# Optimization experiments

Measured on AMD Instinct MI355X. Metric: run time of the kernel, lower is better.

The kernel has to match this reference:

```python
import jax, jax.numpy as jnp
import numpy as np

N_NODES = 100000
IN_FEAT, HID, OUT_FEAT, GRID = 128, 64, 40, 8
N_EDGES = 1600000


def spmm(row, col, w, x):
    # out[i] = sum_{e: row[e]==i} w[e] * x[col[e]]
    return jax.ops.segment_sum(w[:, None] * x[col], row, num_segments=N_NODES)


def kan_layer(x, coeff):
    # coeff: [2, out, in, grid]; Fourier KAN: y[b,j] = sum_{i,k} cos(k x_bi) C0[j,i,k] + sin(k x_bi) C1[j,i,k]
    grid = coeff.shape[-1]
    k = jnp.arange(1, grid + 1, dtype=x.dtype)  # [G]
    ang = x[:, :, None] * k  # [N, in, G]
    y = jnp.einsum('bik,jik->bj', jnp.cos(ang), coeff[0])
    y = y + jnp.einsum('bik,jik->bj', jnp.sin(ang), coeff[1])
    return y


def setup_inputs() -> dict:
    key = jax.random.key(0)
    ks = jax.random.split(key, 8)
    scale = 1.0 / (np.sqrt(HID) * np.sqrt(GRID))
    return {
        'x': jax.random.normal(ks[0], (N_NODES, IN_FEAT), dtype=jnp.float32),
        'edge_row': jax.random.randint(ks[1], (N_EDGES,), 0, N_NODES),
        'edge_col': jax.random.randint(ks[2], (N_EDGES,), 0, N_NODES),
        'edge_weight': jax.random.uniform(ks[3], (N_EDGES,), dtype=jnp.float32),
        'W_in': jax.random.normal(ks[4], (IN_FEAT, HID), dtype=jnp.float32) / np.sqrt(IN_FEAT),
        'b_in': jnp.zeros((HID,), dtype=jnp.float32),
        'coeffs1': jax.random.normal(ks[5], (2, HID, HID, GRID), dtype=jnp.float32) * scale,
        'coeffs2': jax.random.normal(ks[6], (2, HID, HID, GRID), dtype=jnp.float32) * scale,
        'W_out': jax.random.normal(ks[7], (HID, OUT_FEAT), dtype=jnp.float32) / np.sqrt(HID),
    }


def reference(x, edge_row, edge_col, edge_weight, W_in, b_in, coeffs1, coeffs2, W_out):
    h = x @ W_in + b_in                                  # lin_in
    h = kan_layer(spmm(edge_row, edge_col, edge_weight, h), coeffs1)
    h = kan_layer(spmm(edge_row, edge_col, edge_weight, h), coeffs2)
    out = h @ W_out                                      # final bias-free linear
    return jax.nn.log_softmax(out, axis=-1)
```

## Files before the change

kernel.cpp:

```cpp
#include <hip/hip_runtime.h>
#include <hip/hip_bf16.h>
#include <string.h>


#define N_NODES 100000
#define IN_FEAT 128
#define HID 64
#define OUT_FEAT 40
#define NGRID 8
#define N_EDGES 1600000
#define NELEM (N_NODES * HID)

#define NB 98
#define CAP 18432
#define BCHUNK 4096
#define BIN_BLOCKS ((N_EDGES + BCHUNK - 1) / BCHUNK)
#define NTILES ((N_NODES + 63) / 64)

using short8 = __attribute__((ext_vector_type(8))) short;
using floatx4 = __attribute__((ext_vector_type(4))) float;
using uintx4 = __attribute__((ext_vector_type(4))) unsigned;

#define GLOAD_LDS16(gp, lp)                                                   \
  __builtin_amdgcn_global_load_lds(                                           \
      (const __attribute__((address_space(1))) unsigned*)(gp),                \
      (__attribute__((address_space(3))) unsigned*)(lp), 16, 0, 0)

__device__ __forceinline__ unsigned pack_bf16x2(float c, float s) {
  unsigned uc = __float_as_uint(c);
  unsigned us = __float_as_uint(s);
  uc += 0x7fffu + ((uc >> 16) & 1u);
  us += 0x7fffu + ((us >> 16) & 1u);
  return (uc >> 16) | (us & 0xffff0000u);
}

__device__ __forceinline__ unsigned cvtpk_bf16x2(float c, float s) {
  __hip_bfloat162 p = __float22bfloat162_rn(make_float2(c, s));
  unsigned r;
  memcpy(&r, &p, 4);
  return r;
}

__global__ __launch_bounds__(256) void prep_kernel(
    const float* __restrict__ x, const float* __restrict__ W,
    const float* __restrict__ b, float* __restrict__ h,
    const float* __restrict__ c1, const float* __restrict__ c2,
    unsigned* __restrict__ Brep1, unsigned* __restrict__ Brep2,
    int* __restrict__ btail) {
  __shared__ __align__(16) float xs[16 * IN_FEAT];
  int t = threadIdx.x;
  int nb = blockIdx.x;
  if (nb < 6250) {
    const float4* xsrc = (const float4*)(x + (size_t)nb * 16 * IN_FEAT);
    float4* xd = (float4*)xs;
    xd[t] = xsrc[t];
    xd[t + 256] = xsrc[t + 256];
    __syncthreads();
    int lane = t & 63, wv = t >> 6;
    float bj = b[lane];
    float a0 = bj, a1 = bj, a2 = bj, a3 = bj;
    const float* xr = xs + wv * 4 * IN_FEAT;
    const float* Wj = W + lane;
#pragma unroll 4
    for (int i4 = 0; i4 < 32; i4++) {
      float4 x0 = *(const float4*)(xr + 0 * IN_FEAT + i4 * 4);
      float4 x1 = *(const float4*)(xr + 1 * IN_FEAT + i4 * 4);
      float4 x2 = *(const float4*)(xr + 2 * IN_FEAT + i4 * 4);
      float4 x3 = *(const float4*)(xr + 3 * IN_FEAT + i4 * 4);
      float w0 = Wj[(i4 * 4 + 0) * HID];
      float w1 = Wj[(i4 * 4 + 1) * HID];
      float w2 = Wj[(i4 * 4 + 2) * HID];
      float w3 = Wj[(i4 * 4 + 3) * HID];
      a0 = fmaf(x0.x, w0, a0); a0 = fmaf(x0.y, w1, a0); a0 = fmaf(x0.z, w2, a0); a0 = fmaf(x0.w, w3, a0);
      a1 = fmaf(x1.x, w0, a1); a1 = fmaf(x1.y, w1, a1); a1 = fmaf(x1.z, w2, a1); a1 = fmaf(x1.w, w3, a1);
      a2 = fmaf(x2.x, w0, a2); a2 = fmaf(x2.y, w1, a2); a2 = fmaf(x2.z, w2, a2); a2 = fmaf(x2.w, w3, a2);
      a3 = fmaf(x3.x, w0, a3); a3 = fmaf(x3.y, w1, a3); a3 = fmaf(x3.z, w2, a3); a3 = fmaf(x3.w, w3, a3);
    }
    size_t nbase = (size_t)nb * 16 + wv * 4;
    h[(nbase + 0) * HID + lane] = a0;
    h[(nbase + 1) * HID + lane] = a1;
    h[(nbase + 2) * HID + lane] = a2;
    h[(nbase + 3) * HID + lane] = a3;
  } else if (nb < 6506) {
    int rb = nb - 6250;
    const float* coeffs = (rb < 128) ? c1 : c2;
    unsigned* Brep = (rb < 128) ? Brep1 : Brep2;
    int idx = (rb & 127) * 256 + t;
    int ch = idx >> 13;
    int rem = idx & 8191;
    int blk = rem >> 8;
    int jt = blk >> 3, ks = blk & 7;
    int rem2 = rem & 255;
    int ls = rem2 >> 2;
    int quad = ls >> 4, m_n = ls & 15;
    int jj = rem2 & 3;
    int j = jt * 16 + m_n;
    int r = ks >> 1, km1 = ((ks & 1) << 2) | jj;
    int i = ch * 16 + quad * 4 + r;
    int ws = i * 8 + km1;
    float cc0 = coeffs[(size_t)j * 512 + ws];
    float cc1 = coeffs[32768 + (size_t)j * 512 + ws];
    Brep[idx] = pack_bf16x2(cc0, cc1);
  } else {
    if (t < NB) btail[t] = t * CAP;
  }
}

__global__ __launch_bounds__(256) void bin_kernel(
    const int* __restrict__ row, const int* __restrict__ col,
    const float* __restrict__ w, int* __restrict__ btail,
    uint2* __restrict__ pack1) {
  __shared__ __align__(16) uint2 stage[BCHUNK];
  __shared__ int bcnt[NB];
  __shared__ int lbase[NB];
  __shared__ int gbase[NB];
  __shared__ int lcur[NB];
  __shared__ int sc[128];
  int t = threadIdx.x;
  int e0 = blockIdx.x * BCHUNK;
  if (t < NB) bcnt[t] = 0;
  __syncthreads();
  int rloc[16];
#pragma unroll
  for (int q = 0; q < 16; q++) {
    int e = e0 + q * 256 + t;
    int r = (e < N_EDGES) ? row[e] : -1;
    rloc[q] = r;
    if (r >= 0) atomicAdd(&bcnt[r >> 10], 1);
  }
  __syncthreads();
  int c = (t < NB) ? bcnt[t] : 0;
  if (t < 128) sc[t] = c;
  __syncthreads();
  int v = c;
#pragma unroll
  for (int off = 1; off < 128; off <<= 1) {
    int add = (t >= off && t < 128) ? sc[t - off] : 0;
    __syncthreads();
    if (t < 128) sc[t] = v = v + add;
    __syncthreads();
  }
  if (t < NB) {
    lbase[t] = v - c;
    lcur[t] = v - c;
    gbase[t] = atomicAdd(&btail[t], c);
  }
  __syncthreads();
#pragma unroll
  for (int q = 0; q < 16; q++) {
    int e = e0 + q * 256 + t;
    int r = rloc[q];
    if (r >= 0) {
      int p = atomicAdd(&lcur[r >> 10], 1);
      unsigned key = ((unsigned)(r & 1023) << 17) | (unsigned)col[e];
      stage[p] = make_uint2(key, __float_as_uint(w[e]));
    }
  }
  __syncthreads();
  int wv = t >> 6, lane = t & 63;
  for (int b = wv; b < NB; b += 4) {
    int len = bcnt[b], src = lbase[b];
    uint2* dst = pack1 + (size_t)gbase[b];
    for (int i = lane; i < len; i += 64)
      dst[i] = stage[src + i];
  }
}

__global__ __launch_bounds__(256) void bucket_finalize_kernel(
    const int* __restrict__ btail, const uint2* __restrict__ pack1,
    int* __restrict__ rowptr, uint2* __restrict__ pack2) {
  __shared__ int rcnt[1024];
  __shared__ int sc[256];
  __shared__ int binfo[2];
  int b = blockIdx.x, t = threadIdx.x;
  if (t < NB) sc[t] = btail[t] - t * CAP;
  rcnt[t] = 0; rcnt[t + 256] = 0; rcnt[t + 512] = 0; rcnt[t + 768] = 0;
  __syncthreads();
  if (t == 0) {
    int base = 0;
    for (int i = 0; i < b; i++) base += sc[i];
    binfo[0] = base;
    binfo[1] = sc[b];
  }
  __syncthreads();
  int base = binfo[0], len = binfo[1];
  const uint2* rec = pack1 + (size_t)b * CAP;
  for (int i = t; i < len; i += 256)
    atomicAdd(&rcnt[rec[i].x >> 17], 1);
  __syncthreads();
  int c0 = rcnt[4 * t], c1 = rcnt[4 * t + 1], c2 = rcnt[4 * t + 2], c3 = rcnt[4 * t + 3];
  int s4 = c0 + c1 + c2 + c3;
  sc[t] = s4;
  __syncthreads();
  int v = s4;
#pragma unroll
  for (int off = 1; off < 256; off <<= 1) {
    int add = (t >= off) ? sc[t - off] : 0;
    __syncthreads();
    sc[t] = v = v + add;
    __syncthreads();
  }
  int excl = v - s4;
  int p0 = base + excl;
  int p1 = p0 + c0, p2 = p1 + c1, p3 = p2 + c2;
  int r0 = (b << 10) + 4 * t;
  if (r0 + 0 < N_NODES) rowptr[r0 + 0] = p0;
  if (r0 + 1 < N_NODES) rowptr[r0 + 1] = p1;
  if (r0 + 2 < N_NODES) rowptr[r0 + 2] = p2;
  if (r0 + 3 < N_NODES) rowptr[r0 + 3] = p3;
  rcnt[4 * t] = p0; rcnt[4 * t + 1] = p1; rcnt[4 * t + 2] = p2; rcnt[4 * t + 3] = p3;
  __syncthreads();
  for (int i = t; i < len; i += 256) {
    uint2 p = rec[i];
    int pos = atomicAdd(&rcnt[p.x >> 17], 1);
    pack2[pos] = make_uint2(p.x & 0x1FFFFu, p.y);
  }
  if (b == NB - 1 && t == 0) rowptr[N_NODES] = N_EDGES;
}

template <int DO_FINAL>
__global__ __launch_bounds__(256, 4) void fused_spmm_kan_kernel(
    const int* __restrict__ rowptr, const uint2* __restrict__ pack,
    const float* __restrict__ hin, const unsigned* __restrict__ Brep,
    float* __restrict__ outp, const float* __restrict__ Wout) {
  __shared__ __align__(16) unsigned Bs[2][2048];
  __shared__ __align__(16) float s_tile[64 * 64];
  int t = threadIdx.x;
  int lane = t & 63, wv = t >> 6;
  int nb = blockIdx.x;
  const char* Gb = (const char*)Brep;

#pragma unroll
  for (int i = 0; i < 2; i++) {
    int c = wv + 4 * i;
    GLOAD_LDS16(Gb + c * 1024 + lane * 16, (char*)&Bs[0][0] + c * 1024);
  }

  {
    int rpi = nb * 64 + wv * 16 + lane;
    int rp = 0;
    if (lane < 17) rp = rowptr[rpi < N_NODES ? rpi : N_NODES];
    int slot = lane >> 4, f4 = lane & 15;
    const float4* h4 = (const float4*)hin;
    const unsigned long long* packq = (const unsigned long long*)pack;
    for (int i = 0; i < 16; i++) {
      int beg = __shfl(rp, i), end = __shfl(rp, i + 1);
      float4 v = make_float4(0.f, 0.f, 0.f, 0.f);
      for (int e = beg; e < end; e += 16) {
        int i0 = e + slot, i1 = i0 + 4, i2 = i0 + 8, i3 = i0 + 12;
        int c0 = i0 < end ? i0 : end - 1;
        int c1 = i1 < end ? i1 : end - 1;
        int c2 = i2 < end ? i2 : end - 1;
        int c3 = i3 < end ? i3 : end - 1;
        unsigned long long p0 = __builtin_nontemporal_load(packq + c0);
        unsigned long long p1 = __builtin_nontemporal_load(packq + c1);
        unsigned long long p2 = __builtin_nontemporal_load(packq + c2);
        unsigned long long p3 = __builtin_nontemporal_load(packq + c3);
        float4 h0 = h4[(size_t)(unsigned)p0 * 16 + f4];
        float4 h1 = h4[(size_t)(unsigned)p1 * 16 + f4];
        float4 h2 = h4[(size_t)(unsigned)p2 * 16 + f4];
        float4 h3 = h4[(size_t)(unsigned)p3 * 16 + f4];
        float w0 = (i0 < end) ? __uint_as_float((unsigned)(p0 >> 32)) : 0.f;
        float w1 = (i1 < end) ? __uint_as_float((unsigned)(p1 >> 32)) : 0.f;
        float w2 = (i2 < end) ? __uint_as_float((unsigned)(p2 >> 32)) : 0.f;
        float w3 = (i3 < end) ? __uint_as_float((unsigned)(p3 >> 32)) : 0.f;
        v.x = fmaf(w0, h0.x, v.x); v.y = fmaf(w0, h0.y, v.y);
        v.z = fmaf(w0, h0.z, v.z); v.w = fmaf(w0, h0.w, v.w);
        v.x = fmaf(w1, h1.x, v.x); v.y = fmaf(w1, h1.y, v.y);
        v.z = fmaf(w1, h1.z, v.z); v.w = fmaf(w1, h1.w, v.w);
        v.x = fmaf(w2, h2.x, v.x); v.y = fmaf(w2, h2.y, v.y);
        v.z = fmaf(w2, h2.z, v.z); v.w = fmaf(w2, h2.w, v.w);
        v.x = fmaf(w3, h3.x, v.x); v.y = fmaf(w3, h3.y, v.y);
        v.z = fmaf(w3, h3.z, v.z); v.w = fmaf(w3, h3.w, v.w);
      }
#pragma unroll
      for (int off = 16; off < 64; off <<= 1) {
        v.x += __shfl_xor(v.x, off);
        v.y += __shfl_xor(v.y, off);
        v.z += __shfl_xor(v.z, off);
        v.w += __shfl_xor(v.w, off);
      }
      if (slot == 0)
        *(float4*)&s_tile[(wv * 16 + i) * 64 + f4 * 4] = v;
    }
  }
  __syncthreads();

  int m_n = lane & 15, quad = lane >> 4;
  int node_sub = wv * 16 + m_n;
  float4 sv[4];
#pragma unroll
  for (int ch = 0; ch < 4; ch++)
    sv[ch] = *(const float4*)&s_tile[node_sub * 64 + ch * 16 + quad * 4];

  floatx4 acc[4];
#pragma unroll
  for (int jt = 0; jt < 4; jt++) acc[jt] = (floatx4){0.f, 0.f, 0.f, 0.f};
  short8 afr[8];

#pragma unroll
  for (int q = 0; q < 16; q++) {
    asm volatile("s_waitcnt vmcnt(0)" ::: "memory");
    __syncthreads();
    if (q < 15) {
      int qq = q + 1;
      const char* gsrc = Gb + (qq >> 2) * 32768 + (qq & 3) * 8192;
      char* ldst = (char*)&Bs[qq & 1][0];
#pragma unroll
      for (int i = 0; i < 2; i++) {
        int c = wv + 4 * i;
        GLOAD_LDS16(gsrc + c * 1024 + lane * 16, ldst + c * 1024);
      }
    }
    if ((q & 3) == 0) {
      int ch = q >> 2;
      float ss[4] = {sv[ch].x, sv[ch].y, sv[ch].z, sv[ch].w};
#pragma unroll
      for (int r = 0; r < 4; r++) {
        float s1, c1;
        __sincosf(ss[r], &s1, &c1);
        float ck = c1, sk = s1;
        unsigned wbuf[8];
#pragma unroll
        for (int km1 = 0; km1 < 8; km1++) {
          wbuf[km1] = cvtpk_bf16x2(ck, sk);
          float cn = fmaf(ck, c1, -sk * s1);
          float sn = fmaf(sk, c1, ck * s1);
          ck = cn; sk = sn;
        }
        uintx4 lo = (uintx4){wbuf[0], wbuf[1], wbuf[2], wbuf[3]};
        uintx4 hi = (uintx4){wbuf[4], wbuf[5], wbuf[6], wbuf[7]};
        memcpy(&afr[2 * r], &lo, 16);
        memcpy(&afr[2 * r + 1], &hi, 16);
      }
    }
    const char* Bb = (const char*)&Bs[q & 1][0];
    int jt = q & 3;
#pragma unroll
    for (int ks = 0; ks < 8; ks++) {
      short8 bf = *reinterpret_cast<const short8*>(Bb + ks * 1024 + lane * 16);
      acc[jt] = __builtin_amdgcn_mfma_f32_16x16x32_bf16(afr[ks], bf, acc[jt], 0, 0, 0);
    }
  }

  if (DO_FINAL == 0) {
#pragma unroll
    for (int jt = 0; jt < 4; jt++) {
#pragma unroll
      for (int reg = 0; reg < 4; reg++) {
        int node = nb * 64 + wv * 16 + quad * 4 + reg;
        if (node < N_NODES)
          outp[(size_t)node * HID + jt * 16 + m_n] = acc[jt][reg];
      }
    }
  } else {
#pragma unroll
    for (int jt = 0; jt < 4; jt++) {
#pragma unroll
      for (int reg = 0; reg < 4; reg++)
        s_tile[(wv * 16 + quad * 4 + reg) * 64 + jt * 16 + m_n] = acc[jt][reg];
    }
    __syncthreads();
    bool jvalid = lane < OUT_FEAT;
    int jc = jvalid ? lane : 0;
    float wl[HID];
#pragma unroll
    for (int i2 = 0; i2 < HID; i2++)
      wl[i2] = Wout[i2 * OUT_FEAT + jc];
    int nwbase = nb * 64 + wv * 16;
    for (int ns = 0; ns < 16; ns += 2) {
      const float* h0p = &s_tile[(wv * 16 + ns) * 64];
      const float* h1p = h0p + 64;
      float d0 = 0.f, d1 = 0.f;
#pragma unroll
      for (int i4 = 0; i4 < 16; i4++) {
        float4 a = *(const float4*)(h0p + i4 * 4);
        float4 b = *(const float4*)(h1p + i4 * 4);
        d0 = fmaf(a.x, wl[i4 * 4 + 0], d0);  d1 = fmaf(b.x, wl[i4 * 4 + 0], d1);
        d0 = fmaf(a.y, wl[i4 * 4 + 1], d0);  d1 = fmaf(b.y, wl[i4 * 4 + 1], d1);
        d0 = fmaf(a.z, wl[i4 * 4 + 2], d0);  d1 = fmaf(b.z, wl[i4 * 4 + 2], d1);
        d0 = fmaf(a.w, wl[i4 * 4 + 3], d0);  d1 = fmaf(b.w, wl[i4 * 4 + 3], d1);
      }
      float m0 = jvalid ? d0 : -1e30f;
      float m1 = jvalid ? d1 : -1e30f;
#pragma unroll
      for (int off = 32; off; off >>= 1) {
        m0 = fmaxf(m0, __shfl_xor(m0, off));
        m1 = fmaxf(m1, __shfl_xor(m1, off));
      }
      float e0 = jvalid ? expf(d0 - m0) : 0.f;
      float e1 = jvalid ? expf(d1 - m1) : 0.f;
      float s0 = e0, s1 = e1;
#pragma unroll
      for (int off = 32; off; off >>= 1) {
        s0 += __shfl_xor(s0, off);
        s1 += __shfl_xor(s1, off);
      }
      float l0 = m0 + logf(s0);
      float l1 = m1 + logf(s1);
      int n0 = nwbase + ns, n1 = n0 + 1;
      if (jvalid) {
        if (n0 < N_NODES) outp[(size_t)n0 * OUT_FEAT + lane] = d0 - l0;
        if (n1 < N_NODES) outp[(size_t)n1 * OUT_FEAT + lane] = d1 - l1;
      }
    }
  }
}

extern "C" void kernel_launch(void* const* d_in, const int* in_sizes, int n_in,
                              void* d_out, int out_size, void* d_ws, size_t ws_size,
                              hipStream_t stream) {
  (void)in_sizes; (void)n_in; (void)out_size; (void)ws_size;
  const float* x    = (const float*)d_in[0];
  const int*   erow = (const int*)d_in[1];
  const int*   ecol = (const int*)d_in[2];
  const float* ew   = (const float*)d_in[3];
  const float* W_in = (const float*)d_in[4];
  const float* b_in = (const float*)d_in[5];
  const float* c1   = (const float*)d_in[6];
  const float* c2   = (const float*)d_in[7];
  const float* Wout = (const float*)d_in[8];
  float* out = (float*)d_out;

  float* h0 = (float*)d_ws;
  float* h1 = h0 + NELEM;

  unsigned* xw     = (unsigned*)(void*)x;
  unsigned* Brep1  = xw;
  unsigned* Brep2  = xw + 32768;
  int*      btail  = (int*)(xw + 65536);
  int*      rowptr = (int*)(xw + 66048);
  uint2*    pack1  = (uint2*)(xw + 262144);
  uint2*    pack2  = (uint2*)(xw + 3932160);

  prep_kernel<<<6507, 256, 0, stream>>>(x, W_in, b_in, h0, c1, c2,
                                        Brep1, Brep2, btail);
  bin_kernel<<<BIN_BLOCKS, 256, 0, stream>>>(erow, ecol, ew, btail, pack1);
  bucket_finalize_kernel<<<NB, 256, 0, stream>>>(btail, pack1, rowptr, pack2);

  fused_spmm_kan_kernel<0><<<NTILES, 256, 0, stream>>>(
      rowptr, pack2, h0, Brep1, h1, nullptr);
  fused_spmm_kan_kernel<1><<<NTILES, 256, 0, stream>>>(
      rowptr, pack2, h1, Brep2, out, Wout);
}
```

Measured before the change: 417.7 us.

## Drop LDS tile from SpMM-KAN kernel and split final projection into separate kernel

The fused SpMM+KAN kernel no longer stages gathered rows in a 16KB shared tile. Each wave instead redistributes the reduced values into MFMA operand registers with shuffles, which frees LDS and lets launch bounds rise from 4 to 8 blocks per CU. The final W_out projection and log_softmax move into a separate kernel, so the main kernel carries no extra register or LDS pressure from the epilogue. The cost is one extra launch plus a write and read of the 100000x64 hidden activations, and more shuffle instructions inside the node loop.

```diff
diff --git a/kernel.cpp b/kernel.cpp
--- a/kernel.cpp
+++ b/kernel.cpp
@@ -218,17 +218,16 @@
   if (b == NB - 1 && t == 0) rowptr[N_NODES] = N_EDGES;
 }
 
-template <int DO_FINAL>
-__global__ __launch_bounds__(256, 4) void fused_spmm_kan_kernel(
+__global__ __launch_bounds__(256, 8) void fused_spmm_kan_kernel(
     const int* __restrict__ rowptr, const uint2* __restrict__ pack,
     const float* __restrict__ hin, const unsigned* __restrict__ Brep,
-    float* __restrict__ outp, const float* __restrict__ Wout) {
+    float* __restrict__ hout) {
   __shared__ __align__(16) unsigned Bs[2][2048];
-  __shared__ __align__(16) float s_tile[64 * 64];
   int t = threadIdx.x;
   int lane = t & 63, wv = t >> 6;
   int nb = blockIdx.x;
   const char* Gb = (const char*)Brep;
+  int m_n = lane & 15, quad = lane >> 4;
 
 #pragma unroll
   for (int i = 0; i < 2; i++) {
@@ -236,18 +235,18 @@
     GLOAD_LDS16(Gb + c * 1024 + lane * 16, (char*)&Bs[0][0] + c * 1024);
   }
 
+  float4 sv[4];
   {
     int rpi = nb * 64 + wv * 16 + lane;
     int rp = 0;
     if (lane < 17) rp = rowptr[rpi < N_NODES ? rpi : N_NODES];
-    int slot = lane >> 4, f4 = lane & 15;
     const float4* h4 = (const float4*)hin;
     const unsigned long long* packq = (const unsigned long long*)pack;
     for (int i = 0; i < 16; i++) {
       int beg = __shfl(rp, i), end = __shfl(rp, i + 1);
       float4 v = make_float4(0.f, 0.f, 0.f, 0.f);
       for (int e = beg; e < end; e += 16) {
-        int i0 = e + slot, i1 = i0 + 4, i2 = i0 + 8, i3 = i0 + 12;
+        int i0 = e + quad, i1 = i0 + 4, i2 = i0 + 8, i3 = i0 + 12;
         int c0 = i0 < end ? i0 : end - 1;
         int c1 = i1 < end ? i1 : end - 1;
         int c2 = i2 < end ? i2 : end - 1;
@@ -256,10 +255,10 @@
         unsigned long long p1 = __builtin_nontemporal_load(packq + c1);
         unsigned long long p2 = __builtin_nontemporal_load(packq + c2);
         unsigned long long p3 = __builtin_nontemporal_load(packq + c3);
-        float4 h0 = h4[(size_t)(unsigned)p0 * 16 + f4];
-        float4 h1 = h4[(size_t)(unsigned)p1 * 16 + f4];
-        float4 h2 = h4[(size_t)(unsigned)p2 * 16 + f4];
-        float4 h3 = h4[(size_t)(unsigned)p3 * 16 + f4];
+        float4 h0 = h4[(size_t)(unsigned)p0 * 16 + m_n];
+        float4 h1 = h4[(size_t)(unsigned)p1 * 16 + m_n];
+        float4 h2 = h4[(size_t)(unsigned)p2 * 16 + m_n];
+        float4 h3 = h4[(size_t)(unsigned)p3 * 16 + m_n];
         float w0 = (i0 < end) ? __uint_as_float((unsigned)(p0 >> 32)) : 0.f;
         float w1 = (i1 < end) ? __uint_as_float((unsigned)(p1 >> 32)) : 0.f;
         float w2 = (i2 < end) ? __uint_as_float((unsigned)(p2 >> 32)) : 0.f;
@@ -280,18 +279,17 @@
         v.z += __shfl_xor(v.z, off);
         v.w += __shfl_xor(v.w, off);
       }
-      if (slot == 0)
-        *(float4*)&s_tile[(wv * 16 + i) * 64 + f4 * 4] = v;
-    }
-  }
-  __syncthreads();
-
-  int m_n = lane & 15, quad = lane >> 4;
-  int node_sub = wv * 16 + m_n;
-  float4 sv[4];
-#pragma unroll
-  for (int ch = 0; ch < 4; ch++)
-    sv[ch] = *(const float4*)&s_tile[node_sub * 64 + ch * 16 + quad * 4];
+#pragma unroll
+      for (int ch = 0; ch < 4; ch++) {
+        int src = ch * 4 + quad;
+        float gx = __shfl(v.x, src);
+        float gy = __shfl(v.y, src);
+        float gz = __shfl(v.z, src);
+        float gw = __shfl(v.w, src);
+        if (m_n == i) sv[ch] = make_float4(gx, gy, gz, gw);
+      }
+    }
+  }
 
   floatx4 acc[4];
 #pragma unroll
@@ -343,66 +341,74 @@
     }
   }
 
-  if (DO_FINAL == 0) {
-#pragma unroll
-    for (int jt = 0; jt < 4; jt++) {
-#pragma unroll
-      for (int reg = 0; reg < 4; reg++) {
-        int node = nb * 64 + wv * 16 + quad * 4 + reg;
-        if (node < N_NODES)
-          outp[(size_t)node * HID + jt * 16 + m_n] = acc[jt][reg];
-      }
-    }
-  } else {
-#pragma unroll
-    for (int jt = 0; jt < 4; jt++) {
-#pragma unroll
-      for (int reg = 0; reg < 4; reg++)
-        s_tile[(wv * 16 + quad * 4 + reg) * 64 + jt * 16 + m_n] = acc[jt][reg];
-    }
-    __syncthreads();
-    bool jvalid = lane < OUT_FEAT;
-    int jc = jvalid ? lane : 0;
-    float wl[HID];
-#pragma unroll
-    for (int i2 = 0; i2 < HID; i2++)
-      wl[i2] = Wout[i2 * OUT_FEAT + jc];
-    int nwbase = nb * 64 + wv * 16;
-    for (int ns = 0; ns < 16; ns += 2) {
-      const float* h0p = &s_tile[(wv * 16 + ns) * 64];
-      const float* h1p = h0p + 64;
-      float d0 = 0.f, d1 = 0.f;
-#pragma unroll
-      for (int i4 = 0; i4 < 16; i4++) {
-        float4 a = *(const float4*)(h0p + i4 * 4);
-        float4 b = *(const float4*)(h1p + i4 * 4);
-        d0 = fmaf(a.x, wl[i4 * 4 + 0], d0);  d1 = fmaf(b.x, wl[i4 * 4 + 0], d1);
-        d0 = fmaf(a.y, wl[i4 * 4 + 1], d0);  d1 = fmaf(b.y, wl[i4 * 4 + 1], d1);
-        d0 = fmaf(a.z, wl[i4 * 4 + 2], d0);  d1 = fmaf(b.z, wl[i4 * 4 + 2], d1);
-        d0 = fmaf(a.w, wl[i4 * 4 + 3], d0);  d1 = fmaf(b.w, wl[i4 * 4 + 3], d1);
-      }
-      float m0 = jvalid ? d0 : -1e30f;
-      float m1 = jvalid ? d1 : -1e30f;
-#pragma unroll
-      for (int off = 32; off; off >>= 1) {
-        m0 = fmaxf(m0, __shfl_xor(m0, off));
-        m1 = fmaxf(m1, __shfl_xor(m1, off));
-      }
-      float e0 = jvalid ? expf(d0 - m0) : 0.f;
-      float e1 = jvalid ? expf(d1 - m1) : 0.f;
-      float s0 = e0, s1 = e1;
-#pragma unroll
-      for (int off = 32; off; off >>= 1) {
-        s0 += __shfl_xor(s0, off);
-        s1 += __shfl_xor(s1, off);
-      }
-      float l0 = m0 + logf(s0);
-      float l1 = m1 + logf(s1);
-      int n0 = nwbase + ns, n1 = n0 + 1;
-      if (jvalid) {
-        if (n0 < N_NODES) outp[(size_t)n0 * OUT_FEAT + lane] = d0 - l0;
-        if (n1 < N_NODES) outp[(size_t)n1 * OUT_FEAT + lane] = d1 - l1;
-      }
+#pragma unroll
+  for (int jt = 0; jt < 4; jt++) {
+#pragma unroll
+    for (int reg = 0; reg < 4; reg++) {
+      int node = nb * 64 + wv * 16 + quad * 4 + reg;
+      if (node < N_NODES)
+        hout[(size_t)node * HID + jt * 16 + m_n] = acc[jt][reg];
+    }
+  }
+}
+
+__global__ __launch_bounds__(256, 2) void final_kernel(
+    const float* __restrict__ h, const float* __restrict__ Wout,
+    float* __restrict__ out) {
+  __shared__ __align__(16) float hs[64 * HID];
+  int t = threadIdx.x;
+  int lane = t & 63, wv = t >> 6;
+  int nb = blockIdx.x;
+  bool jvalid = lane < OUT_FEAT;
+  int jc = jvalid ? lane : 0;
+
+  float wl[HID];
+#pragma unroll
+  for (int i = 0; i < HID; i++)
+    wl[i] = Wout[i * OUT_FEAT + jc];
+
+  const float4* hsrc = (const float4*)(h + (size_t)nb * 64 * HID);
+  float4* hd = (float4*)hs;
+#pragma unroll
+  for (int q = 0; q < 4; q++)
+    hd[q * 256 + t] = hsrc[q * 256 + t];
+  __syncthreads();
+
+  int nwbase = nb * 64 + wv * 16;
+  for (int ns = 0; ns < 16; ns += 2) {
+    const float* h0 = hs + (wv * 16 + ns) * HID;
+    const float* h1 = h0 + HID;
+    float d0 = 0.f, d1 = 0.f;
+#pragma unroll
+    for (int i4 = 0; i4 < 16; i4++) {
+      float4 a = *(const float4*)(h0 + i4 * 4);
+      float4 b = *(const float4*)(h1 + i4 * 4);
+      d0 = fmaf(a.x, wl[i4 * 4 + 0], d0);  d1 = fmaf(b.x, wl[i4 * 4 + 0], d1);
+      d0 = fmaf(a.y, wl[i4 * 4 + 1], d0);  d1 = fmaf(b.y, wl[i4 * 4 + 1], d1);
+      d0 = fmaf(a.z, wl[i4 * 4 + 2], d0);  d1 = fmaf(b.z, wl[i4 * 4 + 2], d1);
+      d0 = fmaf(a.w, wl[i4 * 4 + 3], d0);  d1 = fmaf(b.w, wl[i4 * 4 + 3], d1);
+    }
+    float m0 = jvalid ? d0 : -1e30f;
+    float m1 = jvalid ? d1 : -1e30f;
+#pragma unroll
+    for (int off = 32; off; off >>= 1) {
+      m0 = fmaxf(m0, __shfl_xor(m0, off));
+      m1 = fmaxf(m1, __shfl_xor(m1, off));
+    }
+    float e0 = jvalid ? expf(d0 - m0) : 0.f;
+    float e1 = jvalid ? expf(d1 - m1) : 0.f;
+    float s0 = e0, s1 = e1;
+#pragma unroll
+    for (int off = 32; off; off >>= 1) {
+      s0 += __shfl_xor(s0, off);
+      s1 += __shfl_xor(s1, off);
+    }
+    float l0 = m0 + logf(s0);
+    float l1 = m1 + logf(s1);
+    int n0 = nwbase + ns, n1 = n0 + 1;
+    if (jvalid) {
+      if (n0 < N_NODES) out[(size_t)n0 * OUT_FEAT + lane] = d0 - l0;
+      if (n1 < N_NODES) out[(size_t)n1 * OUT_FEAT + lane] = d1 - l1;
     }
   }
 }
@@ -438,8 +444,9 @@
   bin_kernel<<<BIN_BLOCKS, 256, 0, stream>>>(erow, ecol, ew, btail, pack1);
   bucket_finalize_kernel<<<NB, 256, 0, stream>>>(btail, pack1, rowptr, pack2);
 
-  fused_spmm_kan_kernel<0><<<NTILES, 256, 0, stream>>>(
-      rowptr, pack2, h0, Brep1, h1, nullptr);
-  fused_spmm_kan_kernel<1><<<NTILES, 256, 0, stream>>>(
-      rowptr, pack2, h1, Brep2, out, Wout);
-}
+  fused_spmm_kan_kernel<<<NTILES, 256, 0, stream>>>(
+      rowptr, pack2, h0, Brep1, h1);
+  fused_spmm_kan_kernel<<<NTILES, 256, 0, stream>>>(
+      rowptr, pack2, h1, Brep2, h0);
+  final_kernel<<<NTILES, 256, 0, stream>>>(h0, Wout, out);
+}
```

New measurement: 702.4 us. +68.1%, slower.
